# Kernel optimization log

Measured on AMD Instinct MI355X. Metric: run time of the kernel, lower is better.

## Reference

```python
import jax, jax.numpy as jnp
import numpy as np

N = 50000            # nodes
E = 800000           # random edges (self loops added in reference, per PyG default)
D_IN, D1, D2, D_OUT = 256, 128, 64, 40
SLOPE = 0.2          # GATv2Conv default negative_slope


def _glorot(key, shape):
    fan_in, fan_out = shape[0], shape[-1]
    s = jnp.sqrt(6.0 / (fan_in + fan_out))
    return jax.random.uniform(key, shape, jnp.float32, -s, s)


def setup_inputs() -> dict:
    key = jax.random.key(0)
    ks = jax.random.split(key, 16)
    inp = {
        "x": jax.random.normal(ks[0], (N, D_IN), jnp.float32),
        "edge_index": jax.random.randint(ks[1], (2, E), 0, N),
    }
    dims = [(D_IN, D1), (D1, D2), (D2, D_OUT)]
    k = 2
    for i, (di, do) in enumerate(dims, 1):
        inp[f"W{i}l"] = _glorot(ks[k], (di, do)); k += 1
        inp[f"W{i}r"] = _glorot(ks[k], (di, do)); k += 1
        inp[f"b{i}l"] = jnp.zeros((do,), jnp.float32)
        inp[f"b{i}r"] = jnp.zeros((do,), jnp.float32)
        inp[f"a{i}"]  = _glorot(ks[k], (do,));    k += 1
        inp[f"c{i}"]  = jnp.zeros((do,), jnp.float32)
    return inp


def _gatv2(x, src, dst, Wl, bl, Wr, br, att, bias):
    # GATv2Conv, heads=1: lin_l on source nodes, lin_r on target nodes
    xl = x @ Wl + bl                     # [N, do] source transform
    xr = x @ Wr + br                     # [N, do] target transform
    e = jax.nn.leaky_relu(xl[src] + xr[dst], SLOPE)   # [Etot, do]
    logits = e @ att                     # [Etot]
    # segment softmax over incoming edges of each dst node
    m = jax.ops.segment_max(logits, dst, num_segments=N)
    ex = jnp.exp(logits - m[dst])
    denom = jax.ops.segment_sum(ex, dst, num_segments=N)
    alpha = ex / denom[dst]              # [Etot]
    out = jax.ops.segment_sum(alpha[:, None] * xl[src], dst, num_segments=N)
    return out + bias


def reference(x, edge_index,
              W1l, W1r, b1l, b1r, a1, c1,
              W2l, W2r, b2l, b2r, a2, c2,
              W3l, W3r, b3l, b3r, a3, c3):
    loop = jnp.arange(N, dtype=edge_index.dtype)
    src = jnp.concatenate([edge_index[0], loop])   # add_self_loops=True
    dst = jnp.concatenate([edge_index[1], loop])
    h = jax.nn.relu(_gatv2(x, src, dst, W1l, b1l, W1r, b1r, a1, c1))
    h = jax.nn.relu(_gatv2(h, src, dst, W2l, b2l, W2r, b2r, a2, c2))
    h = _gatv2(h, src, dst, W3l, b3l, W3r, b3r, a3, c3)
    return jax.nn.log_softmax(h, axis=1)
```

## Files before the change

### kernel.cpp

```cpp
#include <hip/hip_runtime.h>
#include <math.h>

#define NN 50000
#define NE 800000
#define SLOPE 0.2f
#define NEGX (-1e30f)
#define CH 8192

typedef _Float16 h8 __attribute__((ext_vector_type(8)));
typedef _Float16 h2 __attribute__((ext_vector_type(2)));
typedef float f8 __attribute__((ext_vector_type(8)));
typedef float v4f __attribute__((ext_vector_type(4)));

__device__ __forceinline__ h8 hzero(){ h8 z = {0,0,0,0,0,0,0,0}; return z; }
__device__ __forceinline__ f8 fzero(){ f8 z = {0,0,0,0,0,0,0,0}; return z; }

__device__ __forceinline__ void pack_one(const float* __restrict__ W,
                                         _Float16* __restrict__ Wp,
                                         int DO, int K, int NT, int t){
  int KC = K >> 5;
  if (t >= NT * KC * 64) return;
  int lane = t & 63;
  int rest = t >> 6;
  int c  = rest % KC;
  int nt = rest / KC;
  int col = nt * 16 + (lane & 15);
  int k0  = c * 32 + ((lane >> 4) << 3);
  _Float16 o[8];
#pragma unroll
  for (int j = 0; j < 8; j++){
    float v = (col < DO) ? W[(k0 + j) * DO + col] : 0.f;
    o[j] = (_Float16)v;
  }
  *(ulonglong2*)(Wp + (size_t)t * 8) = *(ulonglong2*)o;
}

__global__ __launch_bounds__(256) void k_pack_hist(
    const float* W1l, const float* W1r, const float* W2l,
    const float* W2r, const float* W3l, const float* W3r,
    _Float16* p1l, _Float16* p1r, _Float16* p2l,
    _Float16* p2r, _Float16* p3l, _Float16* p3r,
    const int* __restrict__ ei, int* __restrict__ gbp,
    int* __restrict__ deg, int* __restrict__ row_ptr){
  __shared__ int h[256];
  int b = blockIdx.x, t = threadIdx.x;
  if (b < 44){
    if      (b < 16) pack_one(W1l, p1l, 128, 256, 8, (b     ) * 256 + t);
    else if (b < 32) pack_one(W1r, p1r, 128, 256, 8, (b - 16) * 256 + t);
    else if (b < 36) pack_one(W2l, p2l,  64, 128, 4, (b - 32) * 256 + t);
    else if (b < 40) pack_one(W2r, p2r,  64, 128, 4, (b - 36) * 256 + t);
    else if (b < 42) pack_one(W3l, p3l,  40,  64, 3, (b - 40) * 256 + t);
    else             pack_one(W3r, p3r,  40,  64, 3, (b - 42) * 256 + t);
  } else {
    int hb = b - 44;
    if (hb == 0 && t == 0) row_ptr[NN] = NE;
    h[t] = 0;
    __syncthreads();
    int e0 = hb * 12500;
    for (int i = t; i < 12500; i += 256){
      int d = ei[NE + e0 + i];
      atomicAdd(&h[d >> 8], 1);
      atomicAdd(&deg[d], 1);
    }
    __syncthreads();
    gbp[hb * 256 + t] = h[t];
  }
}

__device__ __forceinline__ void gemm_body(
    int bb,
    const float* __restrict__ X,
    const _Float16* __restrict__ Wpl, const float* __restrict__ bl,
    const _Float16* __restrict__ Wpr, const float* __restrict__ br,
    _Float16* __restrict__ Yl, _Float16* __restrict__ Yr)
{
  constexpr int K = 256, DO = 128;
  constexpr int KC = K / 32;
  constexpr int NT = DO / 16;
  int lane = threadIdx.x & 63;
  int wv   = threadIdx.x >> 6;
  int row0 = (bb * 4 + wv) * 16;
  int arow = lane & 15;
  int koff = lane >> 4;
  int lrow = row0 + arow;
  int crow = (lrow < NN) ? lrow : 0;

  h8 afrag[KC];
  const float* Xr = X + (size_t)crow * K + koff * 8;
#pragma unroll
  for (int c = 0; c < KC; c++){
    float4 v0 = *reinterpret_cast<const float4*>(Xr + c * 32);
    float4 v1 = *reinterpret_cast<const float4*>(Xr + c * 32 + 4);
    h8 a;
    a[0]=(_Float16)v0.x; a[1]=(_Float16)v0.y; a[2]=(_Float16)v0.z; a[3]=(_Float16)v0.w;
    a[4]=(_Float16)v1.x; a[5]=(_Float16)v1.y; a[6]=(_Float16)v1.z; a[7]=(_Float16)v1.w;
    afrag[c] = a;
  }

#pragma unroll
  for (int side = 0; side < 2; side++){
    const _Float16* Wp = side ? Wpr : Wpl;
    const float* bias = side ? br : bl;
    _Float16* Y = side ? Yr : Yl;
#pragma unroll
    for (int nt = 0; nt < NT; nt++){
      v4f acc = {0.f, 0.f, 0.f, 0.f};
#pragma unroll
      for (int c = 0; c < KC; c++){
        h8 b = *reinterpret_cast<const h8*>(Wp + (size_t)((nt * KC + c) * 64 + lane) * 8);
        acc = __builtin_amdgcn_mfma_f32_16x16x32_f16(afrag[c], b, acc, 0, 0, 0);
      }
      int col = nt * 16 + arow;
      if (col < DO){
        float bv = bias[col];
        int rbase = row0 + koff * 4;
#pragma unroll
        for (int r = 0; r < 4; r++){
          int orow = rbase + r;
          if (orow < NN) Y[(size_t)orow * DO + col] = (_Float16)(acc[r] + bv);
        }
      }
    }
  }
}

__global__ __launch_bounds__(256, 4) void k_fused2(
    const int* __restrict__ ei, const int* __restrict__ gbp,
    int* __restrict__ bcur, int* __restrict__ base,
    unsigned* __restrict__ pk_out,
    const int* __restrict__ deg, int* __restrict__ dcnt,
    const float* __restrict__ X,
    const _Float16* __restrict__ Wpl, const float* __restrict__ bl,
    const _Float16* __restrict__ Wpr, const float* __restrict__ br,
    _Float16* __restrict__ Yl, _Float16* __restrict__ Yr)
{
  __shared__ unsigned smem[CH + 512];
  int b = blockIdx.x, t = threadIdx.x;
  if (b < 98){
    unsigned* pk = smem;
    int* h = (int*)(smem + CH);
    int* s = h + 256;
    int v = 0;
#pragma unroll 8
    for (int i = 0; i < 64; i++) v += gbp[i * 256 + t];
    s[t] = v; __syncthreads();
    for (int off = 1; off < 256; off <<= 1){
      int a = (t >= off) ? s[t - off] : 0;
      __syncthreads(); s[t] += a; __syncthreads();
    }
    int ex = s[t] - v;
    if (b == 0){
      base[t] = ex;
      if (t == 255) base[256] = NE;
    }
    h[t] = 0;
    __syncthreads();
    int e0 = b * CH;
    int n = NE - e0; if (n > CH) n = CH;
    for (int i = t; i < n; i += 256){
      int e = e0 + i;
      int sN = ei[e], d = ei[NE + e];
      pk[i] = (unsigned)sN | ((unsigned)(d & 255) << 16) | ((unsigned)(d >> 8) << 24);
      atomicAdd(&h[d >> 8], 1);
    }
    __syncthreads();
    int c = h[t];
    if (c) h[t] = ex + atomicAdd(&bcur[t], c);
    __syncthreads();
    for (int i = t; i < n; i += 256){
      unsigned u = pk[i];
      int pos = atomicAdd(&h[u >> 24], 1);
      pk_out[pos] = u;
    }
  } else if (b < 294){
    int* lh = (int*)smem;
    lh[t] = 0;
    __syncthreads();
    int node = (b - 98) * 256 + t;
    if (node < NN){
      int dg = deg[node];
      atomicAdd(&lh[dg < 255 ? dg : 255], 1);
    }
    __syncthreads();
    if (lh[t]) atomicAdd(&dcnt[t], lh[t]);
  } else {
    gemm_body(b - 294, X, Wpl, bl, Wpr, br, Yl, Yr);
  }
}

__global__ __launch_bounds__(256) void k_bcsr_perm(
    const unsigned* __restrict__ pk, const int* __restrict__ base,
    int* __restrict__ row_ptr, int* __restrict__ csr_src,
    const int* __restrict__ dcnt, int* __restrict__ dcur,
    int* __restrict__ perm){
  __shared__ int h[256], s[256];
  int t = threadIdx.x;
  int b = blockIdx.x;
  int lo = base[b], hi = base[b + 1];
  h[t] = 0;
  __syncthreads();
  for (int i = lo + t; i < hi; i += 256)
    atomicAdd(&h[(pk[i] >> 16) & 255], 1);
  __syncthreads();
  int v = h[t];
  s[t] = v; __syncthreads();
  for (int off = 1; off < 256; off <<= 1){
    int a = (t >= off) ? s[t - off] : 0;
    __syncthreads(); s[t] += a; __syncthreads();
  }
  int ex = lo + s[t] - v;
  int node = b * 256 + t;
  if (node < NN) row_ptr[node] = ex;
  h[t] = ex;
  __syncthreads();
  for (int i = lo + t; i < hi; i += 256){
    unsigned u = pk[i];
    int pos = atomicAdd(&h[(u >> 16) & 255], 1);
    csr_src[pos] = (int)(u & 0xFFFFu);
  }
  __syncthreads();
  s[t] = 0;
  int dv = dcnt[t];
  __syncthreads();
  int bin = v < 255 ? v : 255;
  if (node < NN) atomicAdd(&s[bin], 1);
  h[t] = dv;
  __syncthreads();
  for (int off = 1; off < 256; off <<= 1){
    int a = (t >= off) ? h[t - off] : 0;
    __syncthreads(); h[t] += a; __syncthreads();
  }
  int dbase = h[t] - dv;
  int c = s[t];
  int bp = c ? (dbase + atomicAdd(&dcur[t], c)) : 0;
  __syncthreads();
  s[t] = bp;
  __syncthreads();
  if (node < NN){
    int pos = atomicAdd(&s[bin], 1);
    perm[pos] = node;
  }
}

template<int CTRL>
__device__ __forceinline__ float dppmv(float v){
  int x = __builtin_amdgcn_update_dpp(0, __float_as_int(v), CTRL, 0xF, 0xF, true);
  return __int_as_float(x);
}

template<int LPG>
__device__ __forceinline__ float gsum(float v){
  v += dppmv<177>(v);
  v += dppmv<78>(v);
  if (LPG >= 8)  v += dppmv<0x141>(v);
  if (LPG == 16) v += dppmv<0x140>(v);
  return v;
}
template<int LPG>
__device__ __forceinline__ void gsum2(float& a, float& b){
  a = gsum<LPG>(a);
  b = gsum<LPG>(b);
}
template<int LPG>
__device__ __forceinline__ void gsum4(float& a, float& b, float& c, float& d){
  a = gsum<LPG>(a);
  b = gsum<LPG>(b);
  c = gsum<LPG>(c);
  d = gsum<LPG>(d);
}
template<int LPG>
__device__ __forceinline__ float gmax(float v){
  v = fmaxf(v, dppmv<177>(v));
  v = fmaxf(v, dppmv<78>(v));
  if (LPG >= 8)  v = fmaxf(v, dppmv<0x141>(v));
  if (LPG == 16) v = fmaxf(v, dppmv<0x140>(v));
  return v;
}

__device__ __forceinline__ float edge_logit(h8 x, h8 xrv, h8 attv){
  h8 t = x + xrv;
  h8 l = __builtin_elementwise_max(t, t * (_Float16)SLOPE);
  const h2* lp = (const h2*)&l;
  const h2* ap = (const h2*)&attv;
  float d = __builtin_amdgcn_fdot2(lp[0], ap[0], 0.f, false);
  d = __builtin_amdgcn_fdot2(lp[1], ap[1], d, false);
  d = __builtin_amdgcn_fdot2(lp[2], ap[2], d, false);
  d = __builtin_amdgcn_fdot2(lp[3], ap[3], d, false);
  return d;
}

__device__ __forceinline__ void fmix(f8& acc, h8 x, float w){
#pragma unroll
  for (int j = 0; j < 8; j++) acc[j] = fmaf((float)x[j], w, acc[j]);
}

template<int DO, int LPG, int DO2>
__global__ __launch_bounds__(256) void agg_gemm(
    const _Float16* __restrict__ xl, const _Float16* __restrict__ xr,
    const int* __restrict__ csr_src, const int* __restrict__ row_ptr,
    const int* __restrict__ perm,
    const float* __restrict__ att, const float* __restrict__ bias,
    const _Float16* __restrict__ Wpl2, const float* __restrict__ bl2,
    const _Float16* __restrict__ Wpr2, const float* __restrict__ br2,
    _Float16* __restrict__ Yl, _Float16* __restrict__ Yr)
{
  constexpr int G = 64 / LPG;
  constexpr int NPB = 4 * G;
  constexpr int LK = DO + 8;
  constexpr int KC2 = DO / 32;
  constexpr int NT2 = (DO2 + 15) / 16;
  constexpr int MT = NPB / 16;
  __shared__ _Float16 hs[NPB * LK];
  __shared__ int nodeOf[NPB];

  int tid  = threadIdx.x;
  int lane = tid & 63;
  int wid  = tid >> 6;

  unsigned seg = (unsigned)(blockIdx.x * 1021u) % gridDim.x;
  if (tid < NPB){
    int idx = seg * NPB + tid;
    nodeOf[tid] = (idx < NN) ? perm[idx] : NN;
  }
  __syncthreads();

  int g = lane / LPG, p = lane % LPG;
  int nodeLocal = wid * G + g;
  int node = nodeOf[nodeLocal];
  int cbase = p * 8;
  bool nvalid = node < NN;
  int nodeC = nvalid ? node : 0;

  h8 attv, xrv, xlv;
  {
    float4 a0 = *reinterpret_cast<const float4*>(att + cbase);
    float4 a1 = *reinterpret_cast<const float4*>(att + cbase + 4);
    attv[0]=(_Float16)a0.x; attv[1]=(_Float16)a0.y; attv[2]=(_Float16)a0.z; attv[3]=(_Float16)a0.w;
    attv[4]=(_Float16)a1.x; attv[5]=(_Float16)a1.y; attv[6]=(_Float16)a1.z; attv[7]=(_Float16)a1.w;
    xrv = *reinterpret_cast<const h8*>(xr + nodeC * DO + cbase);
    xlv = *reinterpret_cast<const h8*>(xl + nodeC * DO + cbase);
  }
  float s = gsum<LPG>(edge_logit(xlv, xrv, attv));
  float wS = __expf(s);
  float denA = wS, denB = 0.f;
  f8 accA = fzero(), accB = fzero();
  fmix(accA, xlv, wS);

  int e0 = row_ptr[nodeC];
  int e1 = nvalid ? row_ptr[nodeC + 1] : e0;
  int e = e0;
  for (; e + 3 < e1; e += 4){
    int s0 = csr_src[e],     s1 = csr_src[e + 1];
    int s2 = csr_src[e + 2], s3 = csr_src[e + 3];
    h8 x0 = *reinterpret_cast<const h8*>(xl + s0 * DO + cbase);
    h8 x1 = *reinterpret_cast<const h8*>(xl + s1 * DO + cbase);
    h8 x2 = *reinterpret_cast<const h8*>(xl + s2 * DO + cbase);
    h8 x3 = *reinterpret_cast<const h8*>(xl + s3 * DO + cbase);
    float p0 = edge_logit(x0, xrv, attv);
    float p1 = edge_logit(x1, xrv, attv);
    float p2 = edge_logit(x2, xrv, attv);
    float p3 = edge_logit(x3, xrv, attv);
    gsum4<LPG>(p0, p1, p2, p3);
    float w0 = __expf(p0), w1 = __expf(p1);
    float w2 = __expf(p2), w3 = __expf(p3);
    denA += w0 + w2; denB += w1 + w3;
    fmix(accA, x0, w0);
    fmix(accB, x1, w1);
    fmix(accA, x2, w2);
    fmix(accB, x3, w3);
  }
  for (; e + 1 < e1; e += 2){
    int sA = csr_src[e], sB = csr_src[e + 1];
    h8 xA = *reinterpret_cast<const h8*>(xl + sA * DO + cbase);
    h8 xB = *reinterpret_cast<const h8*>(xl + sB * DO + cbase);
    float pA = edge_logit(xA, xrv, attv);
    float pB = edge_logit(xB, xrv, attv);
    gsum2<LPG>(pA, pB);
    float wA = __expf(pA), wB = __expf(pB);
    denA += wA; denB += wB;
    fmix(accA, xA, wA);
    fmix(accB, xB, wB);
  }
  if (e < e1){
    int sA = csr_src[e];
    h8 xA = *reinterpret_cast<const h8*>(xl + sA * DO + cbase);
    float pA = gsum<LPG>(edge_logit(xA, xrv, attv));
    float w = __expf(pA);
    denA += w;
    fmix(accA, xA, w);
  }

  {
    float inv = 1.0f / (denA + denB);
    f8 sum = (accA + accB) * inv;
    float4 b0 = *reinterpret_cast<const float4*>(bias + cbase);
    float4 b1 = *reinterpret_cast<const float4*>(bias + cbase + 4);
    f8 bv = {b0.x, b0.y, b0.z, b0.w, b1.x, b1.y, b1.z, b1.w};
    sum += bv;
    sum = __builtin_elementwise_max(sum, fzero());
    *reinterpret_cast<h8*>(&hs[nodeLocal * LK + cbase]) = __builtin_convertvector(sum, h8);
  }
  __syncthreads();

  int arow = lane & 15;
  int koff = lane >> 4;
  int mt = (MT == 1) ? 0 : (wid >> 1);
  h8 afrag[KC2];
#pragma unroll
  for (int c = 0; c < KC2; c++)
    afrag[c] = *reinterpret_cast<const h8*>(&hs[(mt * 16 + arow) * LK + koff * 8 + c * 32]);

  int side = wid & 1;
  const _Float16* Wp = side ? Wpr2 : Wpl2;
  const float* bias2 = side ? br2 : bl2;
  _Float16* Y = side ? Yr : Yl;
  int nt_begin = (MT == 1) ? (wid >> 1) * (NT2 / 2) : 0;
  int nt_end   = (MT == 1) ? nt_begin + NT2 / 2 : NT2;
  for (int nt = nt_begin; nt < nt_end; nt++){
    v4f acc = {0.f, 0.f, 0.f, 0.f};
#pragma unroll
    for (int c = 0; c < KC2; c++){
      h8 b = *reinterpret_cast<const h8*>(Wp + (size_t)((nt * KC2 + c) * 64 + lane) * 8);
      acc = __builtin_amdgcn_mfma_f32_16x16x32_f16(afrag[c], b, acc, 0, 0, 0);
    }
    int col = nt * 16 + arow;
    if (col < DO2){
      float bv = bias2[col];
      int lrbase = mt * 16 + koff * 4;
#pragma unroll
      for (int r = 0; r < 4; r++){
        int orow = nodeOf[lrbase + r];
        if (orow < NN) Y[(size_t)orow * DO2 + col] = (_Float16)(acc[r] + bv);
      }
    }
  }
}

template<int DO, int LPG>
__global__ __launch_bounds__(256) void gat_agg_out(
    const _Float16* __restrict__ xl, const _Float16* __restrict__ xr,
    const int* __restrict__ csr_src, const int* __restrict__ row_ptr,
    const int* __restrict__ perm,
    const float* __restrict__ att, const float* __restrict__ bias,
    float* __restrict__ out)
{
  constexpr int G = 64 / LPG;
  constexpr int NPB = 4 * G;
  __shared__ int nodeOf[NPB];
  int tid  = threadIdx.x;
  int lane = tid & 63;
  int wid  = tid >> 6;

  unsigned seg = (unsigned)(blockIdx.x * 1021u) % gridDim.x;
  if (tid < NPB){
    int idx = seg * NPB + tid;
    nodeOf[tid] = (idx < NN) ? perm[idx] : NN;
  }
  __syncthreads();

  int g = lane / LPG;
  int p = lane % LPG;
  int node = nodeOf[wid * G + g];
  bool nvalid = node < NN;
  int nodeC = nvalid ? node : 0;
  int cbase = p * 8;
  bool ok = (cbase < DO);

  h8 attv = hzero(), xrv = hzero(), xlv = hzero();
  if (ok){
    float4 a0 = *reinterpret_cast<const float4*>(att + cbase);
    float4 a1 = *reinterpret_cast<const float4*>(att + cbase + 4);
    attv[0]=(_Float16)a0.x; attv[1]=(_Float16)a0.y; attv[2]=(_Float16)a0.z; attv[3]=(_Float16)a0.w;
    attv[4]=(_Float16)a1.x; attv[5]=(_Float16)a1.y; attv[6]=(_Float16)a1.z; attv[7]=(_Float16)a1.w;
    xrv = *reinterpret_cast<const h8*>(xr + nodeC * DO + cbase);
    xlv = *reinterpret_cast<const h8*>(xl + nodeC * DO + cbase);
  }

  float s = gsum<LPG>(edge_logit(xlv, xrv, attv));
  float wS = __expf(s);
  float denA = wS, denB = 0.f;
  f8 accA = fzero(), accB = fzero();
  fmix(accA, xlv, wS);

  int e0 = row_ptr[nodeC];
  int e1 = nvalid ? row_ptr[nodeC + 1] : e0;
  int e = e0;
  for (; e + 3 < e1; e += 4){
    int s0 = csr_src[e],     s1 = csr_src[e + 1];
    int s2 = csr_src[e + 2], s3 = csr_src[e + 3];
    h8 x0 = ok ? *reinterpret_cast<const h8*>(xl + s0 * DO + cbase) : hzero();
    h8 x1 = ok ? *reinterpret_cast<const h8*>(xl + s1 * DO + cbase) : hzero();
    h8 x2 = ok ? *reinterpret_cast<const h8*>(xl + s2 * DO + cbase) : hzero();
    h8 x3 = ok ? *reinterpret_cast<const h8*>(xl + s3 * DO + cbase) : hzero();
    float p0 = edge_logit(x0, xrv, attv);
    float p1 = edge_logit(x1, xrv, attv);
    float p2 = edge_logit(x2, xrv, attv);
    float p3 = edge_logit(x3, xrv, attv);
    gsum4<LPG>(p0, p1, p2, p3);
    float w0 = __expf(p0), w1 = __expf(p1);
    float w2 = __expf(p2), w3 = __expf(p3);
    denA += w0 + w2; denB += w1 + w3;
    fmix(accA, x0, w0);
    fmix(accB, x1, w1);
    fmix(accA, x2, w2);
    fmix(accB, x3, w3);
  }
  for (; e + 1 < e1; e += 2){
    int sA = csr_src[e], sB = csr_src[e + 1];
    h8 xA = ok ? *reinterpret_cast<const h8*>(xl + sA * DO + cbase) : hzero();
    h8 xB = ok ? *reinterpret_cast<const h8*>(xl + sB * DO + cbase) : hzero();
    float pA = edge_logit(xA, xrv, attv);
    float pB = edge_logit(xB, xrv, attv);
    gsum2<LPG>(pA, pB);
    float wA = __expf(pA), wB = __expf(pB);
    denA += wA; denB += wB;
    fmix(accA, xA, wA);
    fmix(accB, xB, wB);
  }
  if (e < e1){
    int sA = csr_src[e];
    h8 xA = ok ? *reinterpret_cast<const h8*>(xl + sA * DO + cbase) : hzero();
    float pA = gsum<LPG>(edge_logit(xA, xrv, attv));
    float w = __expf(pA);
    denA += w;
    fmix(accA, xA, w);
  }

  float inv = 1.0f / (denA + denB);
  f8 sumv = (accA + accB) * inv;
  float v[8]; float lmax = NEGX;
#pragma unroll
  for (int j = 0; j < 8; j++){
    v[j] = ok ? (sumv[j] + bias[cbase + j]) : NEGX;
    lmax = fmaxf(lmax, v[j]);
  }
  lmax = gmax<LPG>(lmax);
  float lsum = 0.f;
#pragma unroll
  for (int j = 0; j < 8; j++) lsum += __expf(v[j] - lmax);
  lsum = gsum<LPG>(lsum);
  if (ok && nvalid){
    float lg = lmax + __logf(lsum);
    float* op = (float*)out + node * DO + cbase;
    float4 o0, o1;
    o0.x = v[0] - lg; o0.y = v[1] - lg; o0.z = v[2] - lg; o0.w = v[3] - lg;
    o1.x = v[4] - lg; o1.y = v[5] - lg; o1.z = v[6] - lg; o1.w = v[7] - lg;
    *reinterpret_cast<float4*>(op) = o0;
    *reinterpret_cast<float4*>(op + 4) = o1;
  }
}

extern "C" void kernel_launch(void* const* d_in, const int* in_sizes, int n_in,
                              void* d_out, int out_size, void* d_ws, size_t ws_size,
                              hipStream_t stream) {
  const float* x   = (const float*)d_in[0];
  const int*   ei  = (const int*)d_in[1];
  const float* W1l = (const float*)d_in[2];  const float* W1r = (const float*)d_in[3];
  const float* b1l = (const float*)d_in[4];  const float* b1r = (const float*)d_in[5];
  const float* a1  = (const float*)d_in[6];  const float* c1  = (const float*)d_in[7];
  const float* W2l = (const float*)d_in[8];  const float* W2r = (const float*)d_in[9];
  const float* b2l = (const float*)d_in[10]; const float* b2r = (const float*)d_in[11];
  const float* a2  = (const float*)d_in[12]; const float* c2  = (const float*)d_in[13];
  const float* W3l = (const float*)d_in[14]; const float* W3r = (const float*)d_in[15];
  const float* b3l = (const float*)d_in[16]; const float* b3r = (const float*)d_in[17];
  const float* a3  = (const float*)d_in[18]; const float* c3  = (const float*)d_in[19];
  float* outp = (float*)d_out;

  _Float16* xl1 = (_Float16*)d_ws;
  _Float16* xr1 = xl1 + 6400000;
  _Float16* xl2 = xr1 + 6400000;
  _Float16* xr2 = xl2 + 3200000;
  _Float16* xl3 = xr2 + 3200000;
  _Float16* xr3 = xl3 + 2000000;
  _Float16* wp1l = xr3 + 2000000;
  _Float16* wp1r = wp1l + 32768;
  _Float16* wp2l = wp1r + 32768;
  _Float16* wp2r = wp2l + 8192;
  _Float16* wp3l = wp2r + 8192;
  _Float16* wp3r = wp3l + 3072;
  unsigned* pk   = (unsigned*)(wp3r + 3072);
  int* csr_src   = (int*)(pk + NE);
  int* row_ptr   = csr_src + NE;
  int* gbp       = row_ptr + 50001;
  int* base      = gbp + 16384;
  int* bcur      = base + 257;
  int* dcnt      = bcur + 256;
  int* dcur      = dcnt + 256;
  int* deg       = dcur + 256;
  int* perm      = deg + NN;

  const int FB1 = (NN + 15) / 16;
  const int FB2 = (NN + 31) / 32;
  const int AB3 = (NN + 31) / 32;
  const int GB  = (NN + 63) / 64;
  const int SB  = (NE + CH - 1) / CH;
  const int F2  = SB + 196 + GB;

  hipMemsetAsync(bcur, 0, (size_t)(256 * 3 + NN) * sizeof(int), stream);

  k_pack_hist<<<108, 256, 0, stream>>>(W1l, W1r, W2l, W2r, W3l, W3r,
                                       wp1l, wp1r, wp2l, wp2r, wp3l, wp3r,
                                       ei, gbp, deg, row_ptr);

  k_fused2<<<F2, 256, 0, stream>>>(ei, gbp, bcur, base, pk, deg, dcnt,
                                   x, wp1l, b1l, wp1r, b1r, xl1, xr1);

  k_bcsr_perm<<<196, 256, 0, stream>>>(pk, base, row_ptr, csr_src, dcnt, dcur, perm);

  agg_gemm<128,16,64><<<FB1, 256, 0, stream>>>(xl1, xr1, csr_src, row_ptr, perm,
                                               a1, c1, wp2l, b2l, wp2r, b2r, xl2, xr2);

  agg_gemm<64,8,40><<<FB2, 256, 0, stream>>>(xl2, xr2, csr_src, row_ptr, perm,
                                             a2, c2, wp3l, b3l, wp3r, b3r, xl3, xr3);

  gat_agg_out<40,8><<<AB3, 256, 0, stream>>>(xl3, xr3, csr_src, row_ptr, perm, a3, c3, outp);
}
```

Measured before the change: 296.8 us.

## Derive degree histogram from CSR counts instead of global per-edge degree atomics

Removes the per-edge global atomicAdd into a node degree array and the separate degree-histogram blocks. The degree histogram is now built from the per-node counts already computed while building the CSR. The degree-sorted permutation moves into a new kernel that reads degrees from row_ptr, and the hipMemset is replaced by zeroing the counters inside the first kernel. GEMM blocks are also placed first in the fused kernel. This costs one extra kernel launch.

```diff
diff --git a/kernel.cpp b/kernel.cpp
--- a/kernel.cpp
+++ b/kernel.cpp
@@ -41,7 +41,7 @@
     _Float16* p1l, _Float16* p1r, _Float16* p2l,
     _Float16* p2r, _Float16* p3l, _Float16* p3r,
     const int* __restrict__ ei, int* __restrict__ gbp,
-    int* __restrict__ deg, int* __restrict__ row_ptr){
+    int* __restrict__ bcur, int* __restrict__ row_ptr){
   __shared__ int h[256];
   int b = blockIdx.x, t = threadIdx.x;
   if (b < 44){
@@ -54,14 +54,12 @@
   } else {
     int hb = b - 44;
     if (hb == 0 && t == 0) row_ptr[NN] = NE;
+    if (hb == 1){ bcur[t] = 0; bcur[256 + t] = 0; bcur[512 + t] = 0; }
     h[t] = 0;
     __syncthreads();
     int e0 = hb * 12500;
-    for (int i = t; i < 12500; i += 256){
-      int d = ei[NE + e0 + i];
-      atomicAdd(&h[d >> 8], 1);
-      atomicAdd(&deg[d], 1);
-    }
+    for (int i = t; i < 12500; i += 256)
+      atomicAdd(&h[ei[NE + e0 + i] >> 8], 1);
     __syncthreads();
     gbp[hb * 256 + t] = h[t];
   }
@@ -124,11 +122,13 @@
   }
 }
 
+#define GB ((NN + 63) / 64)
+#define SB ((NE + CH - 1) / CH)
+
 __global__ __launch_bounds__(256, 4) void k_fused2(
     const int* __restrict__ ei, const int* __restrict__ gbp,
     int* __restrict__ bcur, int* __restrict__ base,
     unsigned* __restrict__ pk_out,
-    const int* __restrict__ deg, int* __restrict__ dcnt,
     const float* __restrict__ X,
     const _Float16* __restrict__ Wpl, const float* __restrict__ bl,
     const _Float16* __restrict__ Wpr, const float* __restrict__ br,
@@ -136,7 +136,10 @@
 {
   __shared__ unsigned smem[CH + 512];
   int b = blockIdx.x, t = threadIdx.x;
-  if (b < 98){
+  if (b < GB){
+    gemm_body(b, X, Wpl, bl, Wpr, br, Yl, Yr);
+  } else {
+    int sb = b - GB;
     unsigned* pk = smem;
     int* h = (int*)(smem + CH);
     int* s = h + 256;
@@ -149,13 +152,13 @@
       __syncthreads(); s[t] += a; __syncthreads();
     }
     int ex = s[t] - v;
-    if (b == 0){
+    if (sb == 0){
       base[t] = ex;
       if (t == 255) base[256] = NE;
     }
     h[t] = 0;
     __syncthreads();
-    int e0 = b * CH;
+    int e0 = sb * CH;
     int n = NE - e0; if (n > CH) n = CH;
     for (int i = t; i < n; i += 256){
       int e = e0 + i;
@@ -172,27 +175,14 @@
       int pos = atomicAdd(&h[u >> 24], 1);
       pk_out[pos] = u;
     }
-  } else if (b < 294){
-    int* lh = (int*)smem;
-    lh[t] = 0;
-    __syncthreads();
-    int node = (b - 98) * 256 + t;
-    if (node < NN){
-      int dg = deg[node];
-      atomicAdd(&lh[dg < 255 ? dg : 255], 1);
-    }
-    __syncthreads();
-    if (lh[t]) atomicAdd(&dcnt[t], lh[t]);
-  } else {
-    gemm_body(b - 294, X, Wpl, bl, Wpr, br, Yl, Yr);
-  }
-}
-
-__global__ __launch_bounds__(256) void k_bcsr_perm(
-    const unsigned* __restrict__ pk, const int* __restrict__ base,
-    int* __restrict__ row_ptr, int* __restrict__ csr_src,
-    const int* __restrict__ dcnt, int* __restrict__ dcur,
-    int* __restrict__ perm){
+  }
+}
+
+__global__ __launch_bounds__(256) void k_bcsr(const unsigned* __restrict__ pk,
+                                              const int* __restrict__ base,
+                                              int* __restrict__ row_ptr,
+                                              int* __restrict__ csr_src,
+                                              int* __restrict__ dcnt){
   __shared__ int h[256], s[256];
   int t = threadIdx.x;
   int b = blockIdx.x;
@@ -212,32 +202,48 @@
   int node = b * 256 + t;
   if (node < NN) row_ptr[node] = ex;
   h[t] = ex;
-  __syncthreads();
+  s[t] = 0;
+  __syncthreads();
+  if (node < NN) atomicAdd(&s[v < 255 ? v : 255], 1);
+  __syncthreads();
+  if (s[t]) atomicAdd(&dcnt[t], s[t]);
   for (int i = lo + t; i < hi; i += 256){
     unsigned u = pk[i];
     int pos = atomicAdd(&h[(u >> 16) & 255], 1);
     csr_src[pos] = (int)(u & 0xFFFFu);
   }
-  __syncthreads();
-  s[t] = 0;
+}
+
+__global__ __launch_bounds__(256) void k_dscatter(const int* __restrict__ row_ptr,
+                                                  const int* __restrict__ dcnt,
+                                                  int* __restrict__ dcur,
+                                                  int* __restrict__ perm){
+  __shared__ int lh[256], sc[256];
+  int t = threadIdx.x;
+  int node = blockIdx.x * 256 + t;
+  lh[t] = 0;
   int dv = dcnt[t];
   __syncthreads();
-  int bin = v < 255 ? v : 255;
-  if (node < NN) atomicAdd(&s[bin], 1);
-  h[t] = dv;
+  int bin = -1;
+  if (node < NN){
+    int deg = row_ptr[node + 1] - row_ptr[node];
+    bin = deg < 255 ? deg : 255;
+    atomicAdd(&lh[bin], 1);
+  }
+  sc[t] = dv;
   __syncthreads();
   for (int off = 1; off < 256; off <<= 1){
-    int a = (t >= off) ? h[t - off] : 0;
-    __syncthreads(); h[t] += a; __syncthreads();
-  }
-  int dbase = h[t] - dv;
-  int c = s[t];
-  int bp = c ? (dbase + atomicAdd(&dcur[t], c)) : 0;
-  __syncthreads();
-  s[t] = bp;
+    int a = (t >= off) ? sc[t - off] : 0;
+    __syncthreads(); sc[t] += a; __syncthreads();
+  }
+  int gbase = sc[t] - dv;
+  int c = lh[t];
+  int bp = c ? (gbase + atomicAdd(&dcur[t], c)) : 0;
+  __syncthreads();
+  lh[t] = bp;
   __syncthreads();
   if (node < NN){
-    int pos = atomicAdd(&s[bin], 1);
+    int pos = atomicAdd(&lh[bin], 1);
     perm[pos] = node;
   }
 }
@@ -586,26 +592,23 @@
   int* bcur      = base + 257;
   int* dcnt      = bcur + 256;
   int* dcur      = dcnt + 256;
-  int* deg       = dcur + 256;
-  int* perm      = deg + NN;
+  int* perm      = dcur + 256;
 
   const int FB1 = (NN + 15) / 16;
   const int FB2 = (NN + 31) / 32;
   const int AB3 = (NN + 31) / 32;
-  const int GB  = (NN + 63) / 64;
-  const int SB  = (NE + CH - 1) / CH;
-  const int F2  = SB + 196 + GB;
-
-  hipMemsetAsync(bcur, 0, (size_t)(256 * 3 + NN) * sizeof(int), stream);
+  const int F2  = GB + SB;
 
   k_pack_hist<<<108, 256, 0, stream>>>(W1l, W1r, W2l, W2r, W3l, W3r,
                                        wp1l, wp1r, wp2l, wp2r, wp3l, wp3r,
-                                       ei, gbp, deg, row_ptr);
-
-  k_fused2<<<F2, 256, 0, stream>>>(ei, gbp, bcur, base, pk, deg, dcnt,
+                                       ei, gbp, bcur, row_ptr);
+
+  k_fused2<<<F2, 256, 0, stream>>>(ei, gbp, bcur, base, pk,
                                    x, wp1l, b1l, wp1r, b1r, xl1, xr1);
 
-  k_bcsr_perm<<<196, 256, 0, stream>>>(pk, base, row_ptr, csr_src, dcnt, dcur, perm);
+  k_bcsr<<<196, 256, 0, stream>>>(pk, base, row_ptr, csr_src, dcnt);
+
+  k_dscatter<<<196, 256, 0, stream>>>(row_ptr, dcnt, dcur, perm);
 
   agg_gemm<128,16,64><<<FB1, 256, 0, stream>>>(xl1, xr1, csr_src, row_ptr, perm,
                                                a1, c1, wp2l, b2l, wp2r, b2r, xl2, xr2);
```

Result: faster. 269.0 us (-9.4%).
